# Optimization experiments

Measured on AMD Instinct MI355X. Metric: run time of the kernel, lower is better.

Reference implementation:

```python
import jax, jax.numpy as jnp
import numpy as np

NUM_CLASSES = 10000
EMBED_DIM = 512
BATCH = 4096


def setup_inputs() -> dict:
    key = jax.random.key(0)
    k1, k2, k3 = jax.random.split(key, 3)
    x = jax.random.normal(k1, (BATCH, EMBED_DIM), dtype=jnp.float32)
    labels = jax.random.randint(k2, (BATCH,), 0, NUM_CLASSES, dtype=jnp.int64)
    centers = jax.random.normal(k3, (NUM_CLASSES, EMBED_DIM), dtype=jnp.float32)
    return {"x": x, "labels": labels, "centers": centers}


def reference(x, labels, centers):
    # distmat[b, c] = ||x_b||^2 + ||center_c||^2 - 2 <x_b, center_c>   -> (B, C)
    x_sq = jnp.sum(x * x, axis=1, keepdims=True)               # (B, 1)
    c_sq = jnp.sum(centers * centers, axis=1)[None, :]         # (1, C)
    distmat = x_sq + c_sq - 2.0 * jnp.einsum('bd,cd->bc', x, centers)
    # mask: entry where class index equals the sample's label
    mask = (labels[:, None] == jnp.arange(NUM_CLASSES)[None, :]).astype(x.dtype)
    dist = distmat * mask
    # NOTE: clamp is applied to the *masked* matrix, so the (B*C - B) zero
    # entries are clamped up to 1e-12 and included in the sum (faithful to torch).
    loss = jnp.sum(jnp.clip(dist, 1e-12, 1e12)) / x.shape[0]
    return loss
```

## Files before the change

kernel.cpp:

```cpp
#include <hip/hip_runtime.h>


#define BATCH 4096
#define DIM 512
#define NUM_CLASSES 10000
#define ROWS_PER_WAVE 4
#define WAVES_PER_BLOCK 4
#define ROWS_PER_BLOCK (ROWS_PER_WAVE * WAVES_PER_BLOCK)
#define NUM_BLOCKS (BATCH / ROWS_PER_BLOCK)

__global__ __launch_bounds__(256) void center_loss_fused(
    const float* __restrict__ x,
    const int* __restrict__ labels,
    const float* __restrict__ centers,
    float* __restrict__ out)
{
    const int wave = threadIdx.x >> 6;
    const int lane = threadIdx.x & 63;
    const int row0 = blockIdx.x * ROWS_PER_BLOCK + wave * ROWS_PER_WAVE;

    float4 a[ROWS_PER_WAVE][2], b[ROWS_PER_WAVE][2];
    #pragma unroll
    for (int r = 0; r < ROWS_PER_WAVE; ++r) {
        const int row = row0 + r;
        const int lbl = labels[row];
        const float4* xp = (const float4*)(x + (size_t)row * DIM);
        const float4* cp = (const float4*)(centers + (size_t)lbl * DIM);
        a[r][0] = xp[lane];
        a[r][1] = xp[lane + 64];
        b[r][0] = cp[lane];
        b[r][1] = cp[lane + 64];
    }

    float acc[ROWS_PER_WAVE];
    #pragma unroll
    for (int r = 0; r < ROWS_PER_WAVE; ++r) {
        float d, s = 0.0f;
        d = a[r][0].x - b[r][0].x; s += d * d;
        d = a[r][0].y - b[r][0].y; s += d * d;
        d = a[r][0].z - b[r][0].z; s += d * d;
        d = a[r][0].w - b[r][0].w; s += d * d;
        d = a[r][1].x - b[r][1].x; s += d * d;
        d = a[r][1].y - b[r][1].y; s += d * d;
        d = a[r][1].z - b[r][1].z; s += d * d;
        d = a[r][1].w - b[r][1].w; s += d * d;
        acc[r] = s;
    }

    #pragma unroll
    for (int off = 32; off > 0; off >>= 1) {
        #pragma unroll
        for (int r = 0; r < ROWS_PER_WAVE; ++r)
            acc[r] += __shfl_down(acc[r], off, 64);
    }

    __shared__ float s_wave[WAVES_PER_BLOCK];
    if (lane == 0) {
        float w = 0.0f;
        #pragma unroll
        for (int r = 0; r < ROWS_PER_WAVE; ++r)
            w += fminf(fmaxf(acc[r], 1e-12f), 1e12f);
        s_wave[wave] = w;
    }
    __syncthreads();
    if (threadIdx.x == 0) {
        float blk = s_wave[0] + s_wave[1] + s_wave[2] + s_wave[3];
        float v = blk * (1.0f / BATCH);
        if (blockIdx.x == 0) {
            v += (float)(NUM_CLASSES - 1) * 1e-12f;
        }
        atomicAdd(out, v);
    }
}

extern "C" void kernel_launch(void* const* d_in, const int* in_sizes, int n_in,
                              void* d_out, int out_size, void* d_ws, size_t ws_size,
                              hipStream_t stream) {
    const float* x       = (const float*)d_in[0];
    const int*   labels  = (const int*)d_in[1];
    const float* centers = (const float*)d_in[2];
    float* out = (float*)d_out;

    hipMemsetAsync(out, 0, sizeof(float), stream);
    center_loss_fused<<<NUM_BLOCKS, 256, 0, stream>>>(x, labels, centers, out);
}
```

Before: 76.80 us.

## Replace memset and atomics with cooperative grid-sync final reduction

Drops the separate memset launch and the per-block float atomicAdd. Each block now writes its partial sum to workspace, the grid synchronises cooperatively, and block 0 reduces the 256 partials and writes the result once. This removes a launch and atomic contention and makes the sum deterministic. In exchange it adds the cost of a cooperative launch and a grid-wide barrier.

```diff
diff --git a/kernel.cpp b/kernel.cpp
--- a/kernel.cpp
+++ b/kernel.cpp
@@ -1,4 +1,7 @@
 #include <hip/hip_runtime.h>
+#include <hip/hip_cooperative_groups.h>
+
+namespace cg = cooperative_groups;
 
 
 #define BATCH 4096
@@ -9,11 +12,12 @@
 #define ROWS_PER_BLOCK (ROWS_PER_WAVE * WAVES_PER_BLOCK)
 #define NUM_BLOCKS (BATCH / ROWS_PER_BLOCK)
 
-__global__ __launch_bounds__(256) void center_loss_fused(
+__global__ __launch_bounds__(256) void center_loss_coop(
     const float* __restrict__ x,
     const int* __restrict__ labels,
     const float* __restrict__ centers,
-    float* __restrict__ out)
+    float* __restrict__ out,
+    float* __restrict__ partials)
 {
     const int wave = threadIdx.x >> 6;
     const int lane = threadIdx.x & 63;
@@ -63,13 +67,25 @@
         s_wave[wave] = w;
     }
     __syncthreads();
-    if (threadIdx.x == 0) {
-        float blk = s_wave[0] + s_wave[1] + s_wave[2] + s_wave[3];
-        float v = blk * (1.0f / BATCH);
-        if (blockIdx.x == 0) {
-            v += (float)(NUM_CLASSES - 1) * 1e-12f;
+    if (threadIdx.x == 0)
+        partials[blockIdx.x] = s_wave[0] + s_wave[1] + s_wave[2] + s_wave[3];
+
+    cg::this_grid().sync();
+
+    if (blockIdx.x == 0) {
+        float acc2 = (threadIdx.x < NUM_BLOCKS) ? partials[threadIdx.x] : 0.0f;
+        #pragma unroll
+        for (int off = 32; off > 0; off >>= 1)
+            acc2 += __shfl_down(acc2, off, 64);
+
+        __shared__ float s2[WAVES_PER_BLOCK];
+        if (lane == 0) s2[wave] = acc2;
+        __syncthreads();
+        if (threadIdx.x == 0) {
+            double total = (double)s2[0] + (double)s2[1] + (double)s2[2] + (double)s2[3];
+            total += (double)BATCH * (double)(NUM_CLASSES - 1) * 1e-12;
+            out[0] = (float)(total / (double)BATCH);
         }
-        atomicAdd(out, v);
     }
 }
 
@@ -79,8 +95,11 @@
     const float* x       = (const float*)d_in[0];
     const int*   labels  = (const int*)d_in[1];
     const float* centers = (const float*)d_in[2];
-    float* out = (float*)d_out;
+    float* out   = (float*)d_out;
+    float* parts = (float*)d_ws;
 
-    hipMemsetAsync(out, 0, sizeof(float), stream);
-    center_loss_fused<<<NUM_BLOCKS, 256, 0, stream>>>(x, labels, centers, out);
+    void* args[] = { (void*)&x, (void*)&labels, (void*)&centers,
+                     (void*)&out, (void*)&parts };
+    hipLaunchCooperativeKernel((void*)center_loss_coop,
+                               dim3(NUM_BLOCKS), dim3(256), args, 0, stream);
 }
```

Result: slower. 107.6 us (+40.1%).
